# Optimization experiments

Measured on AMD Instinct MI355X. Metric: run time of the kernel, lower is better.

The kernel has to match this reference:

```python
import jax, jax.numpy as jnp
import numpy as np
from math import sqrt

B, L = 2, 1024
D, H, NL, DFF = 768, 12, 2, 3072
V, LCTX, EOS = 50257, 1024, 50256
STD = 0.02


def _ln(x, w, b, eps=1e-5):
    m = x.mean(-1, keepdims=True)
    v = ((x - m) ** 2).mean(-1, keepdims=True)
    return (x - m) * jax.lax.rsqrt(v + eps) * w + b


def setup_inputs() -> dict:
    key = jax.random.key(0)
    ks = jax.random.split(key, 12)
    ids = jax.random.randint(ks[0], (B, L), 0, V)
    # insert eos tokens so the packed-document mask has real segments
    ids = ids.at[:, 255::256].set(EOS)
    n = lambda k, s: STD * jax.random.normal(k, s, jnp.float32)
    return {
        "input_ids": ids,
        "tok_emb": n(ks[1], (V, D)),
        "pos_emb": n(ks[2], (LCTX, D)),
        "qkv_w": n(ks[3], (NL, 3 * D, D)),
        "qkv_b": jnp.zeros((NL, 3 * D), jnp.float32),
        "out_w": n(ks[4], (NL, D, D)),
        "out_b": jnp.zeros((NL, D), jnp.float32),
        "ln1_w": jnp.ones((NL, D), jnp.float32),
        "ln1_b": jnp.zeros((NL, D), jnp.float32),
        "ln2_w": jnp.ones((NL, D), jnp.float32),
        "ln2_b": jnp.zeros((NL, D), jnp.float32),
        "ff1_w": n(ks[5], (NL, DFF, D)),
        "ff1_b": jnp.zeros((NL, DFF), jnp.float32),
        "ff2_w": n(ks[6], (NL, D, DFF)),
        "ff2_b": jnp.zeros((NL, D), jnp.float32),
    }


def _supporters(input_ids):
    # relative position within document + per-batch additive segment-causal mask
    raw = jnp.arange(L)[None, :]                                   # [1,L]
    is_eos = input_ids == EOS
    last_eos = jax.lax.cummax(jnp.where(is_eos, raw, 0), axis=1)   # [B,L]
    rel_idx = raw - last_eos                                       # [B,L]
    seg = jnp.cumsum(is_eos.astype(jnp.int32), axis=1)             # [B,L]
    same = seg[:, :, None] == seg[:, None, :]                      # [B,L,L]
    causal = jnp.tril(jnp.ones((L, L), bool))
    mask = jnp.where(same & causal, 0.0, -jnp.inf).astype(jnp.float32)
    return rel_idx, mask


def _forward(input_ids, tok_emb, pos_emb, qkv_w, qkv_b, out_w, out_b,
             ln1_w, ln1_b, ln2_w, ln2_b, ff1_w, ff1_b, ff2_w, ff2_b):
    rel_idx, mask = _supporters(input_ids)
    x = tok_emb[input_ids] * sqrt(D) + pos_emb[rel_idx]            # [B,L,D]
    hd = D // H
    scale = 1.0 / sqrt(hd)

    def layer(x, p):
        (qw, qb, ow, ob, l1w, l1b, l2w, l2b, f1w, f1b, f2w, f2b) = p
        qkv = x @ qw.T + qb                                        # [B,L,3D]
        q, k, v = jnp.split(qkv, 3, axis=-1)
        q = q.reshape(B, L, H, hd)
        k = k.reshape(B, L, H, hd)
        v = v.reshape(B, L, H, hd)
        scores = jnp.einsum("bqhd,bkhd->bhqk", q, k) * scale + mask[:, None]
        attn = jax.nn.softmax(scores, axis=-1)
        o = jnp.einsum("bhqk,bkhd->bqhd", attn, v).reshape(B, L, D)
        o = o @ ow.T + ob
        x = _ln(x + o, l1w, l1b)                                   # post-norm
        h = jax.nn.gelu(x @ f1w.T + f1b, approximate=False) @ f2w.T + f2b
        x = _ln(x + h, l2w, l2b)
        return x, None

    x, _ = jax.lax.scan(layer, x, (qkv_w, qkv_b, out_w, out_b, ln1_w, ln1_b,
                                   ln2_w, ln2_b, ff1_w, ff1_b, ff2_w, ff2_b))
    return x @ tok_emb.T                                           # tied decoder


def reference(input_ids, tok_emb, pos_emb, qkv_w, qkv_b, out_w, out_b,
              ln1_w, ln1_b, ln2_w, ln2_b, ff1_w, ff1_b, ff2_w, ff2_b):
    return _forward(input_ids, tok_emb, pos_emb, qkv_w, qkv_b, out_w, out_b,
                    ln1_w, ln1_b, ln2_w, ln2_b, ff1_w, ff1_b, ff2_w, ff2_b)
```

## Files before the change

kernel.cpp:

```cpp
#include <hip/hip_runtime.h>
#include <hip/hip_bf16.h>

#define B_ 2
#define L_ 1024
#define D_ 768
#define H_ 12
#define HD_ 64
#define NL_ 2
#define DFF_ 3072
#define V_ 50257
#define EOS_ 50256
#define TD_ (3 * D_)
#define BL_ (B_ * L_)

typedef __attribute__((ext_vector_type(8))) short bf16x8_t;
typedef __attribute__((ext_vector_type(4))) float f32x4_t;

#define AS1 __attribute__((address_space(1)))
#define AS3 __attribute__((address_space(3)))

__device__ __forceinline__ unsigned short f2bf(float f) {
  union { float f; unsigned int i; } c;
  c.f = f;
  unsigned int x = c.i;
  unsigned int lsb = (x >> 16) & 1u;
  x += 0x7fffu + lsb;
  return (unsigned short)(x >> 16);
}

__device__ __forceinline__ void gload_lds16(const void* g, void* l) {
  __builtin_amdgcn_global_load_lds((AS1 void*)(g), (AS3 void*)(l), 16, 0, 0);
}

__global__ void cvt_kernel(const float* __restrict__ in,
                           unsigned short* __restrict__ out, int n4) {
  int i = blockIdx.x * blockDim.x + threadIdx.x;
  if (i >= n4) return;
  f32x4_t v = *(const f32x4_t*)(in + (size_t)i * 4);
  ushort4 o;
  o.x = f2bf(v[0]); o.y = f2bf(v[1]); o.z = f2bf(v[2]); o.w = f2bf(v[3]);
  *(ushort4*)(out + (size_t)i * 4) = o;
}

__global__ void prep_kernel(const int* __restrict__ ids, int* __restrict__ rel) {
  int i = blockIdx.x * blockDim.x + threadIdx.x;
  if (i >= BL_) return;
  int b = i / L_, l = i % L_;
  const int* row = ids + (size_t)b * L_;
  int r = l;
  for (int j = l; j >= 0; --j) {
    if (row[j] == EOS_) { r = l - j; break; }
  }
  rel[i] = r;
}

__global__ void embed_kernel(const int* __restrict__ ids,
                             const float* __restrict__ tok,
                             const float* __restrict__ pos,
                             const int* __restrict__ rel,
                             float* __restrict__ x,
                             unsigned short* __restrict__ xb) {
  int i = blockIdx.x * blockDim.x + threadIdx.x;
  if (i >= BL_ * D_) return;
  int d = i % D_;
  int bl = i / D_;
  int id = ids[bl];
  int r = rel[bl];
  float val = tok[(size_t)id * D_ + d] * 27.712812921102035f +
              pos[(size_t)r * D_ + d];
  x[i] = val;
  xb[i] = f2bf(val);
}

__global__ __launch_bounds__(256) void gemm_bt_lds_kernel(
    const unsigned short* __restrict__ A, const unsigned short* __restrict__ W,
    const float* __restrict__ bias, float* __restrict__ C,
    int M, int N, int K) {
  __shared__ unsigned short As[128 * 64];
  __shared__ unsigned short Bs[128 * 64];

  const int tid = threadIdx.x;
  const int wave = tid >> 6;
  const int lane = tid & 63;
  const int wr = wave >> 1;
  const int wc = wave & 1;
  const int lr = lane & 15;
  const int kq = (lane >> 4) << 3;

  const int nwg = gridDim.x * gridDim.y;
  const int bidl = blockIdx.y * gridDim.x + blockIdx.x;
  const int xcd = bidl & 7;
  const int q8 = nwg >> 3, r8 = nwg & 7;
  const int lin = (xcd < r8 ? xcd * (q8 + 1)
                            : r8 * (q8 + 1) + (xcd - r8) * q8) + (bidl >> 3);
  const int m0 = (lin % gridDim.x) << 7;
  const int n0 = (lin / gridDim.x) << 7;

  const int srow = tid >> 3;
  const int slot = tid & 7;
  const unsigned short* gA[4];
  const unsigned short* gB[4];
#pragma unroll
  for (int p = 0; p < 4; ++p) {
    int row = p * 32 + srow;
    int kblk = (slot ^ (row & 7)) << 3;
    gA[p] = A + (size_t)(m0 + row) * K + kblk;
    int wrow = n0 + row;
    if (wrow >= N) wrow = N - 1;
    gB[p] = W + (size_t)wrow * K + kblk;
  }

  f32x4_t acc[4][4];
#pragma unroll
  for (int i = 0; i < 4; ++i)
#pragma unroll
    for (int j = 0; j < 4; ++j) acc[i][j] = (f32x4_t){0.f, 0.f, 0.f, 0.f};

  const int xmask = (lr & 7) << 4;
  const char* Ab = (const char*)As;
  const char* Bb = (const char*)Bs;

  for (int k0 = 0; k0 < K; k0 += 64) {
    if (k0) __syncthreads();
#pragma unroll
    for (int p = 0; p < 4; ++p) {
      gload_lds16(gA[p] + k0, (char*)As + p * 4096 + wave * 1024);
      gload_lds16(gB[p] + k0, (char*)Bs + p * 4096 + wave * 1024);
    }
    __syncthreads();
#pragma unroll
    for (int ks = 0; ks < 2; ++ks) {
      const int kb = (ks << 6) + (kq << 1);
      bf16x8_t a[4], b[4];
#pragma unroll
      for (int i = 0; i < 4; ++i)
        a[i] = *(const bf16x8_t*)(Ab + (wr * 64 + i * 16 + lr) * 128 +
                                  (kb ^ xmask));
#pragma unroll
      for (int j = 0; j < 4; ++j)
        b[j] = *(const bf16x8_t*)(Bb + (wc * 64 + j * 16 + lr) * 128 +
                                  (kb ^ xmask));
#pragma unroll
      for (int i = 0; i < 4; ++i)
#pragma unroll
        for (int j = 0; j < 4; ++j)
          acc[i][j] =
              __builtin_amdgcn_mfma_f32_16x16x32_bf16(a[i], b[j], acc[i][j],
                                                      0, 0, 0);
    }
  }

  const int crow0 = m0 + wr * 64 + ((lane >> 4) << 2);
#pragma unroll
  for (int i = 0; i < 4; ++i) {
    int crow = crow0 + i * 16;
#pragma unroll
    for (int j = 0; j < 4; ++j) {
      int col = n0 + wc * 64 + j * 16 + lr;
      if (col >= N) continue;
      float bv = bias ? bias[col] : 0.0f;
#pragma unroll
      for (int r = 0; r < 4; ++r)
        C[(size_t)(crow + r) * N + col] = acc[i][j][r] + bv;
    }
  }
}

template <int W_IS_F32>
__global__ __launch_bounds__(256) void gemm_bt_kernel(
    const unsigned short* __restrict__ A, const void* __restrict__ W,
    const float* __restrict__ bias, float* __restrict__ C,
    int M, int N, int K) {
  int wave = threadIdx.x >> 6;
  int lane = threadIdx.x & 63;
  int lr = lane & 15;
  int kq = (lane >> 4) << 3;
  int n0 = blockIdx.x << 6;
  int m0 = blockIdx.y << 6;
  int row = m0 + wave * 16 + lr;

  const unsigned short* arow = A + (size_t)row * K + kq;
  const unsigned short* browb[4];
  const float* browf[4];
#pragma unroll
  for (int nt = 0; nt < 4; ++nt) {
    int col = n0 + nt * 16 + lr;
    if (col >= N) col = N - 1;
    if (W_IS_F32) browf[nt] = (const float*)W + (size_t)col * K + kq;
    else          browb[nt] = (const unsigned short*)W + (size_t)col * K + kq;
  }

  f32x4_t acc[4] = {{0.f, 0.f, 0.f, 0.f},
                    {0.f, 0.f, 0.f, 0.f},
                    {0.f, 0.f, 0.f, 0.f},
                    {0.f, 0.f, 0.f, 0.f}};

  for (int k0 = 0; k0 < K; k0 += 32) {
    bf16x8_t a = *(const bf16x8_t*)(arow + k0);
#pragma unroll
    for (int nt = 0; nt < 4; ++nt) {
      bf16x8_t bfr;
      if (W_IS_F32) {
        f32x4_t w0 = *(const f32x4_t*)(browf[nt] + k0);
        f32x4_t w1 = *(const f32x4_t*)(browf[nt] + k0 + 4);
#pragma unroll
        for (int j = 0; j < 4; ++j) {
          bfr[j]     = (short)f2bf(w0[j]);
          bfr[4 + j] = (short)f2bf(w1[j]);
        }
      } else {
        bfr = *(const bf16x8_t*)(browb[nt] + k0);
      }
      acc[nt] = __builtin_amdgcn_mfma_f32_16x16x32_bf16(a, bfr, acc[nt], 0, 0, 0);
    }
  }

  int crow = m0 + wave * 16 + ((lane >> 4) << 2);
#pragma unroll
  for (int nt = 0; nt < 4; ++nt) {
    int col = n0 + nt * 16 + lr;
    if (col >= N) continue;
    float bv = bias ? bias[col] : 0.0f;
#pragma unroll
    for (int r = 0; r < 4; ++r) {
      float v = acc[nt][r] + bv;
      C[(size_t)(crow + r) * N + col] = v;
    }
  }
}

__global__ __launch_bounds__(256) void attn_mfma_kernel(
    const float* __restrict__ qkv, const int* __restrict__ rel,
    unsigned short* __restrict__ obf) {
  __shared__ __align__(16) unsigned short k_s[64][72];
  __shared__ __align__(16) unsigned short v_s[64][72];
  __shared__ __align__(16) unsigned short p_s[4][16][72];

  const int tid = threadIdx.x;
  const int wave = tid >> 6, lane = tid & 63;
  const int lr = lane & 15, hi = lane >> 4;

  const int bid = blockIdx.x;
  const int qt0 = (bid & 15) << 6;
  const int h = (bid >> 4) % H_;
  const int b = bid / (16 * H_);
  const int boff = b * L_;

  const int qrow = qt0 + wave * 16 + lr;
  const float* qp = qkv + (size_t)(boff + qrow) * TD_ + h * HD_ + hi * 8;
  bf16x8_t aq[2];
#pragma unroll
  for (int ks = 0; ks < 2; ++ks) {
    f32x4_t q0 = *(const f32x4_t*)(qp + ks * 32);
    f32x4_t q1 = *(const f32x4_t*)(qp + ks * 32 + 4);
#pragma unroll
    for (int j = 0; j < 4; ++j) {
      aq[ks][j] = (short)f2bf(q0[j]);
      aq[ks][4 + j] = (short)f2bf(q1[j]);
    }
  }

  int klo_r[4];
#pragma unroll
  for (int r = 0; r < 4; ++r) {
    int qr = qt0 + wave * 16 + hi * 4 + r;
    klo_r[r] = qr - rel[boff + qr];
  }
  const int base0 = ((qt0 - rel[boff + qt0]) >> 6) << 6;

  float m_r[4] = {-1e30f, -1e30f, -1e30f, -1e30f};
  float l_r[4] = {0.f, 0.f, 0.f, 0.f};
  f32x4_t o_acc[4];
#pragma unroll
  for (int dt = 0; dt < 4; ++dt) o_acc[dt] = (f32x4_t){0.f, 0.f, 0.f, 0.f};

  const int skey = tid >> 2;
  const int sdq = (tid & 3) << 4;

  for (int base = base0; base <= qt0 + 63; base += 64) {
    __syncthreads();
    const float* kp = qkv + (size_t)(boff + base + skey) * TD_ + D_ +
                      h * HD_ + sdq;
    f32x4_t k0 = *(const f32x4_t*)(kp);
    f32x4_t k1 = *(const f32x4_t*)(kp + 4);
    f32x4_t k2 = *(const f32x4_t*)(kp + 8);
    f32x4_t k3 = *(const f32x4_t*)(kp + 12);
    bf16x8_t kb0, kb1;
#pragma unroll
    for (int j = 0; j < 4; ++j) {
      kb0[j] = (short)f2bf(k0[j]); kb0[4 + j] = (short)f2bf(k1[j]);
      kb1[j] = (short)f2bf(k2[j]); kb1[4 + j] = (short)f2bf(k3[j]);
    }
    *(bf16x8_t*)&k_s[skey][sdq] = kb0;
    *(bf16x8_t*)&k_s[skey][sdq + 8] = kb1;

    const float* vp = kp + D_;
    f32x4_t v0 = *(const f32x4_t*)(vp);
    f32x4_t v1 = *(const f32x4_t*)(vp + 4);
    f32x4_t v2 = *(const f32x4_t*)(vp + 8);
    f32x4_t v3 = *(const f32x4_t*)(vp + 12);
#pragma unroll
    for (int j = 0; j < 4; ++j) {
      v_s[sdq + j][skey]      = f2bf(v0[j]);
      v_s[sdq + 4 + j][skey]  = f2bf(v1[j]);
      v_s[sdq + 8 + j][skey]  = f2bf(v2[j]);
      v_s[sdq + 12 + j][skey] = f2bf(v3[j]);
    }
    __syncthreads();

    f32x4_t s[4];
#pragma unroll
    for (int tj = 0; tj < 4; ++tj) {
      s[tj] = (f32x4_t){0.f, 0.f, 0.f, 0.f};
#pragma unroll
      for (int ks = 0; ks < 2; ++ks) {
        bf16x8_t kb = *(const bf16x8_t*)&k_s[tj * 16 + lr][ks * 32 + hi * 8];
        s[tj] = __builtin_amdgcn_mfma_f32_16x16x32_bf16(aq[ks], kb, s[tj],
                                                        0, 0, 0);
      }
    }

    float al_r[4];
#pragma unroll
    for (int r = 0; r < 4; ++r) {
      const int qr = qt0 + wave * 16 + hi * 4 + r;
#pragma unroll
      for (int tj = 0; tj < 4; ++tj) {
        int key = base + tj * 16 + lr;
        bool valid = (key >= klo_r[r]) && (key <= qr);
        s[tj][r] = valid ? s[tj][r] * 0.125f : -1e30f;
      }
      float cm = fmaxf(fmaxf(s[0][r], s[1][r]), fmaxf(s[2][r], s[3][r]));
#pragma unroll
      for (int off = 8; off; off >>= 1)
        cm = fmaxf(cm, __shfl_xor(cm, off, 64));
      float mn = fmaxf(m_r[r], cm);
      al_r[r] = __expf(m_r[r] - mn);
      float rs = 0.f;
#pragma unroll
      for (int tj = 0; tj < 4; ++tj) {
        float p = (s[tj][r] < -1e29f) ? 0.f : __expf(s[tj][r] - mn);
        s[tj][r] = p;
        rs += p;
      }
#pragma unroll
      for (int off = 8; off; off >>= 1) rs += __shfl_xor(rs, off, 64);
      l_r[r] = l_r[r] * al_r[r] + rs;
      m_r[r] = mn;
    }

#pragma unroll
    for (int r = 0; r < 4; ++r) {
#pragma unroll
      for (int tj = 0; tj < 4; ++tj)
        p_s[wave][hi * 4 + r][tj * 16 + lr] = f2bf(s[tj][r]);
#pragma unroll
      for (int dt = 0; dt < 4; ++dt) o_acc[dt][r] *= al_r[r];
    }

#pragma unroll
    for (int ks = 0; ks < 2; ++ks) {
      bf16x8_t pa = *(const bf16x8_t*)&p_s[wave][lr][ks * 32 + hi * 8];
#pragma unroll
      for (int dt = 0; dt < 4; ++dt) {
        bf16x8_t vb = *(const bf16x8_t*)&v_s[dt * 16 + lr][ks * 32 + hi * 8];
        o_acc[dt] = __builtin_amdgcn_mfma_f32_16x16x32_bf16(pa, vb, o_acc[dt],
                                                            0, 0, 0);
      }
    }
  }

#pragma unroll
  for (int r = 0; r < 4; ++r) {
    float inv = 1.f / l_r[r];
    int qr = qt0 + wave * 16 + hi * 4 + r;
    unsigned short* op = obf + (size_t)(boff + qr) * D_ + h * HD_ + lr;
#pragma unroll
    for (int dt = 0; dt < 4; ++dt)
      op[dt * 16] = f2bf(o_acc[dt][r] * inv);
  }
}

__device__ __forceinline__ float block_reduce_sum_256(float v, float* sbuf) {
#pragma unroll
  for (int off = 32; off; off >>= 1) v += __shfl_xor(v, off, 64);
  if ((threadIdx.x & 63) == 0) sbuf[threadIdx.x >> 6] = v;
  __syncthreads();
  float r = sbuf[0] + sbuf[1] + sbuf[2] + sbuf[3];
  __syncthreads();
  return r;
}

__global__ __launch_bounds__(256) void add_ln_kernel(
    const float* __restrict__ x, const float* __restrict__ t,
    const float* __restrict__ w, const float* __restrict__ b,
    float* __restrict__ xo, unsigned short* __restrict__ xbo) {
  __shared__ float sbuf[4];
  size_t base = (size_t)blockIdx.x * D_;
  float v[3];
  float s = 0.f;
#pragma unroll
  for (int i = 0; i < 3; ++i) {
    int idx = threadIdx.x + i * 256;
    v[i] = x[base + idx] + t[base + idx];
    s += v[i];
  }
  float mean = block_reduce_sum_256(s, sbuf) * (1.f / D_);
  float vs = 0.f;
#pragma unroll
  for (int i = 0; i < 3; ++i) {
    float d = v[i] - mean;
    vs += d * d;
  }
  float var = block_reduce_sum_256(vs, sbuf) * (1.f / D_);
  float rstd = rsqrtf(var + 1e-5f);
#pragma unroll
  for (int i = 0; i < 3; ++i) {
    int idx = threadIdx.x + i * 256;
    float o = (v[i] - mean) * rstd * w[idx] + b[idx];
    xo[base + idx] = o;
    xbo[base + idx] = f2bf(o);
  }
}

__global__ void gelu_kernel(const float* __restrict__ h,
                            unsigned short* __restrict__ hb, int n) {
  int i = blockIdx.x * blockDim.x + threadIdx.x;
  if (i >= n) return;
  float x = h[i];
  float g = 0.5f * x * (1.f + erff(x * 0.7071067811865476f));
  hb[i] = f2bf(g);
}

extern "C" void kernel_launch(void* const* d_in, const int* in_sizes, int n_in,
                              void* d_out, int out_size, void* d_ws, size_t ws_size,
                              hipStream_t stream) {
  const int* ids       = (const int*)d_in[0];
  const float* tok     = (const float*)d_in[1];
  const float* pos     = (const float*)d_in[2];
  const float* qkv_w   = (const float*)d_in[3];
  const float* qkv_b   = (const float*)d_in[4];
  const float* out_w   = (const float*)d_in[5];
  const float* out_b   = (const float*)d_in[6];
  const float* ln1_w   = (const float*)d_in[7];
  const float* ln1_b   = (const float*)d_in[8];
  const float* ln2_w   = (const float*)d_in[9];
  const float* ln2_b   = (const float*)d_in[10];
  const float* ff1_w   = (const float*)d_in[11];
  const float* ff2_w   = (const float*)d_in[13];
  const float* ff2_b   = (const float*)d_in[14];
  const float* ff1_b   = (const float*)d_in[12];

  char* ws = (char*)d_ws;
  size_t off = 0;
  auto alloc = [&](size_t bytes) {
    void* p = ws + off;
    off = (off + bytes + 255) & ~(size_t)255;
    return p;
  };
  int* rel            = (int*)alloc((size_t)BL_ * 4);
  float* x            = (float*)alloc((size_t)BL_ * D_ * 4);
  unsigned short* xb  = (unsigned short*)alloc((size_t)BL_ * D_ * 2);
  float* big          = (float*)alloc((size_t)BL_ * DFF_ * 4);
  float* qkvbuf       = big;
  float* hbuf         = big;
  unsigned short* obf = (unsigned short*)alloc((size_t)BL_ * D_ * 2);
  float* t            = (float*)alloc((size_t)BL_ * D_ * 4);
  unsigned short* hb  = (unsigned short*)alloc((size_t)BL_ * DFF_ * 2);
  unsigned short* qkvw_b16 = (unsigned short*)alloc((size_t)NL_ * TD_ * D_ * 2);
  unsigned short* outw_b16 = (unsigned short*)alloc((size_t)NL_ * D_ * D_ * 2);
  unsigned short* ff1w_b16 = (unsigned short*)alloc((size_t)NL_ * DFF_ * D_ * 2);
  unsigned short* ff2w_b16 = (unsigned short*)alloc((size_t)NL_ * D_ * DFF_ * 2);
  size_t base_need = off;
  unsigned short* tok_b16 = (unsigned short*)alloc((size_t)V_ * D_ * 2);
  bool have_tok = (off <= ws_size);
  (void)base_need;

  auto cvt = [&](const float* in, unsigned short* out, size_t n) {
    int n4 = (int)(n / 4);
    cvt_kernel<<<(n4 + 255) / 256, 256, 0, stream>>>(in, out, n4);
  };
  cvt(qkv_w, qkvw_b16, (size_t)NL_ * TD_ * D_);
  cvt(out_w, outw_b16, (size_t)NL_ * D_ * D_);
  cvt(ff1_w, ff1w_b16, (size_t)NL_ * DFF_ * D_);
  cvt(ff2_w, ff2w_b16, (size_t)NL_ * D_ * DFF_);
  if (have_tok) cvt(tok, tok_b16, (size_t)V_ * D_);

  prep_kernel<<<(BL_ + 255) / 256, 256, 0, stream>>>(ids, rel);
  embed_kernel<<<(BL_ * D_ + 255) / 256, 256, 0, stream>>>(ids, tok, pos, rel, x, xb);

  auto gemm = [&](const unsigned short* A, const unsigned short* W,
                  const float* bias, float* C, int M, int N, int K) {
    gemm_bt_lds_kernel<<<dim3(M / 128, (N + 127) / 128), 256, 0, stream>>>(
        A, W, bias, C, M, N, K);
  };

  for (int l = 0; l < NL_; ++l) {
    gemm(xb, qkvw_b16 + (size_t)l * TD_ * D_, qkv_b + (size_t)l * TD_, qkvbuf,
         BL_, TD_, D_);
    attn_mfma_kernel<<<B_ * H_ * (L_ / 64), 256, 0, stream>>>(qkvbuf, rel, obf);
    gemm(obf, outw_b16 + (size_t)l * D_ * D_, out_b + (size_t)l * D_, t,
         BL_, D_, D_);
    add_ln_kernel<<<BL_, 256, 0, stream>>>(x, t, ln1_w + l * D_, ln1_b + l * D_, x, xb);
    gemm(xb, ff1w_b16 + (size_t)l * DFF_ * D_, ff1_b + (size_t)l * DFF_, hbuf,
         BL_, DFF_, D_);
    gelu_kernel<<<(BL_ * DFF_ + 255) / 256, 256, 0, stream>>>(hbuf, hb, BL_ * DFF_);
    gemm(hb, ff2w_b16 + (size_t)l * D_ * DFF_, ff2_b + (size_t)l * D_, t,
         BL_, D_, DFF_);
    add_ln_kernel<<<BL_, 256, 0, stream>>>(x, t, ln2_w + l * D_, ln2_b + l * D_, x, xb);
  }

  if (have_tok) {
    gemm(xb, tok_b16, nullptr, (float*)d_out, BL_, V_, D_);
  } else {
    gemm_bt_kernel<1><<<dim3((V_ + 63) / 64, BL_ / 64), 256, 0, stream>>>(
        xb, tok, nullptr, (float*)d_out, BL_, V_, D_);
  }
}
```

Baseline: 1.204 ms.

## Double-buffer LDS tiles in bf16 GEMM and fuse GELU into FF1 epilogue

The LDS GEMM now keeps two shared-memory buffers and issues the global-to-LDS loads for the next K tile before computing on the current one, waiting with vmcnt so memory latency overlaps the MFMA work. Separately, the FF1 GEMM applies exact GELU in its epilogue and writes bf16 directly, which removes the standalone gelu kernel and the fp32 round trip of the hidden activations. The cost is doubled LDS per block (64KB), which may reduce occupancy. The hand-written waitcnt and barriers also depend on the load count per stage staying correct.

```diff
diff --git a/kernel.cpp b/kernel.cpp
--- a/kernel.cpp
+++ b/kernel.cpp
@@ -72,12 +72,13 @@
   xb[i] = f2bf(val);
 }
 
+template <int ACT>
 __global__ __launch_bounds__(256) void gemm_bt_lds_kernel(
     const unsigned short* __restrict__ A, const unsigned short* __restrict__ W,
-    const float* __restrict__ bias, float* __restrict__ C,
+    const float* __restrict__ bias, void* __restrict__ Cv,
     int M, int N, int K) {
-  __shared__ unsigned short As[128 * 64];
-  __shared__ unsigned short Bs[128 * 64];
+  __shared__ unsigned short As[2][128 * 64];
+  __shared__ unsigned short Bs[2][128 * 64];
 
   const int tid = threadIdx.x;
   const int wave = tid >> 6;
@@ -117,17 +118,30 @@
     for (int j = 0; j < 4; ++j) acc[i][j] = (f32x4_t){0.f, 0.f, 0.f, 0.f};
 
   const int xmask = (lr & 7) << 4;
-  const char* Ab = (const char*)As;
-  const char* Bb = (const char*)Bs;
-
-  for (int k0 = 0; k0 < K; k0 += 64) {
-    if (k0) __syncthreads();
+  const int NKT = K >> 6;
+
+  auto stage = [&](int buf, int kt) {
+    const int k0 = kt << 6;
 #pragma unroll
     for (int p = 0; p < 4; ++p) {
-      gload_lds16(gA[p] + k0, (char*)As + p * 4096 + wave * 1024);
-      gload_lds16(gB[p] + k0, (char*)Bs + p * 4096 + wave * 1024);
-    }
-    __syncthreads();
+      gload_lds16(gA[p] + k0, (char*)As[buf] + p * 4096 + wave * 1024);
+      gload_lds16(gB[p] + k0, (char*)Bs[buf] + p * 4096 + wave * 1024);
+    }
+  };
+
+  stage(0, 0);
+  int cur = 0;
+  for (int kt = 0; kt < NKT; ++kt) {
+    if (kt + 1 < NKT) {
+      stage(cur ^ 1, kt + 1);
+      asm volatile("s_waitcnt vmcnt(8)" ::: "memory");
+    } else {
+      asm volatile("s_waitcnt vmcnt(0)" ::: "memory");
+    }
+    __builtin_amdgcn_s_barrier();
+    __builtin_amdgcn_sched_barrier(0);
+    const char* Ab = (const char*)As[cur];
+    const char* Bb = (const char*)Bs[cur];
 #pragma unroll
     for (int ks = 0; ks < 2; ++ks) {
       const int kb = (ks << 6) + (kq << 1);
@@ -148,6 +162,9 @@
               __builtin_amdgcn_mfma_f32_16x16x32_bf16(a[i], b[j], acc[i][j],
                                                       0, 0, 0);
     }
+    __builtin_amdgcn_sched_barrier(0);
+    __builtin_amdgcn_s_barrier();
+    cur ^= 1;
   }
 
   const int crow0 = m0 + wr * 64 + ((lane >> 4) << 2);
@@ -160,8 +177,15 @@
       if (col >= N) continue;
       float bv = bias ? bias[col] : 0.0f;
 #pragma unroll
-      for (int r = 0; r < 4; ++r)
-        C[(size_t)(crow + r) * N + col] = acc[i][j][r] + bv;
+      for (int r = 0; r < 4; ++r) {
+        float v = acc[i][j][r] + bv;
+        if (ACT == 0) {
+          ((float*)Cv)[(size_t)(crow + r) * N + col] = v;
+        } else {
+          float g = 0.5f * v * (1.f + erff(v * 0.7071067811865476f));
+          ((unsigned short*)Cv)[(size_t)(crow + r) * N + col] = f2bf(g);
+        }
+      }
     }
   }
 }
@@ -421,15 +445,6 @@
     xo[base + idx] = o;
     xbo[base + idx] = f2bf(o);
   }
-}
-
-__global__ void gelu_kernel(const float* __restrict__ h,
-                            unsigned short* __restrict__ hb, int n) {
-  int i = blockIdx.x * blockDim.x + threadIdx.x;
-  if (i >= n) return;
-  float x = h[i];
-  float g = 0.5f * x * (1.f + erff(x * 0.7071067811865476f));
-  hb[i] = f2bf(g);
 }
 
 extern "C" void kernel_launch(void* const* d_in, const int* in_sizes, int n_in,
@@ -463,7 +478,6 @@
   unsigned short* xb  = (unsigned short*)alloc((size_t)BL_ * D_ * 2);
   float* big          = (float*)alloc((size_t)BL_ * DFF_ * 4);
   float* qkvbuf       = big;
-  float* hbuf         = big;
   unsigned short* obf = (unsigned short*)alloc((size_t)BL_ * D_ * 2);
   float* t            = (float*)alloc((size_t)BL_ * D_ * 4);
   unsigned short* hb  = (unsigned short*)alloc((size_t)BL_ * DFF_ * 2);
@@ -491,8 +505,8 @@
 
   auto gemm = [&](const unsigned short* A, const unsigned short* W,
                   const float* bias, float* C, int M, int N, int K) {
-    gemm_bt_lds_kernel<<<dim3(M / 128, (N + 127) / 128), 256, 0, stream>>>(
-        A, W, bias, C, M, N, K);
+    gemm_bt_lds_kernel<0><<<dim3(M / 128, (N + 127) / 128), 256, 0, stream>>>(
+        A, W, bias, (void*)C, M, N, K);
   };
 
   for (int l = 0; l < NL_; ++l) {
@@ -502,9 +516,9 @@
     gemm(obf, outw_b16 + (size_t)l * D_ * D_, out_b + (size_t)l * D_, t,
          BL_, D_, D_);
     add_ln_kernel<<<BL_, 256, 0, stream>>>(x, t, ln1_w + l * D_, ln1_b + l * D_, x, xb);
-    gemm(xb, ff1w_b16 + (size_t)l * DFF_ * D_, ff1_b + (size_t)l * DFF_, hbuf,
-         BL_, DFF_, D_);
-    gelu_kernel<<<(BL_ * DFF_ + 255) / 256, 256, 0, stream>>>(hbuf, hb, BL_ * DFF_);
+    gemm_bt_lds_kernel<1><<<dim3(BL_ / 128, DFF_ / 128), 256, 0, stream>>>(
+        xb, ff1w_b16 + (size_t)l * DFF_ * D_, ff1_b + (size_t)l * DFF_,
+        (void*)hb, BL_, DFF_, D_);
     gemm(hb, ff2w_b16 + (size_t)l * D_ * DFF_, ff2_b + (size_t)l * D_, t,
          BL_, D_, DFF_);
     add_ln_kernel<<<BL_, 256, 0, stream>>>(x, t, ln2_w + l * D_, ln2_b + l * D_, x, xb);
```

Measured after the change: 1.262 ms. 1.05x slower.

## Template GEMM tiles, fuse GELU into FF1 epilogue, nontemporal logits stores

Applied to the files above, without the earlier changes.

Templates the LDS GEMM on tile size, activation, and store type. It adds 64x64 tiles for small-N GEMMs (out-proj, FF2) so more workgroups fill the GPU. GELU is fused into the FF1 epilogue, writing bf16 directly, which removes the fp32 intermediate and the separate gelu pass. The large vocab logits GEMM uses nontemporal stores to avoid cache pollution. Smaller tiles lower data reuse per block, and erf in the epilogue adds compute to the GEMM tail.

```diff
diff --git a/kernel.cpp b/kernel.cpp
--- a/kernel.cpp
+++ b/kernel.cpp
@@ -72,12 +72,16 @@
   xb[i] = f2bf(val);
 }
 
-__global__ __launch_bounds__(256) void gemm_bt_lds_kernel(
+template <int BM, int BN, int ACT, int NT>
+__global__ __launch_bounds__(256) void gemm_tile_kernel(
     const unsigned short* __restrict__ A, const unsigned short* __restrict__ W,
-    const float* __restrict__ bias, float* __restrict__ C,
+    const float* __restrict__ bias, void* __restrict__ Cv,
     int M, int N, int K) {
-  __shared__ unsigned short As[128 * 64];
-  __shared__ unsigned short Bs[128 * 64];
+  constexpr int WTM = BM / 2, WTN = BN / 2;
+  constexpr int FM = WTM / 16, FN = WTN / 16;
+  constexpr int PA = BM / 32, PB = BN / 32;
+  __shared__ unsigned short As[BM * 64];
+  __shared__ unsigned short Bs[BN * 64];
 
   const int tid = threadIdx.x;
   const int wave = tid >> 6;
@@ -93,28 +97,33 @@
   const int q8 = nwg >> 3, r8 = nwg & 7;
   const int lin = (xcd < r8 ? xcd * (q8 + 1)
                             : r8 * (q8 + 1) + (xcd - r8) * q8) + (bidl >> 3);
-  const int m0 = (lin % gridDim.x) << 7;
-  const int n0 = (lin / gridDim.x) << 7;
+  const int m0 = (lin % gridDim.x) * BM;
+  const int n0 = (lin / gridDim.x) * BN;
 
   const int srow = tid >> 3;
   const int slot = tid & 7;
-  const unsigned short* gA[4];
-  const unsigned short* gB[4];
-#pragma unroll
-  for (int p = 0; p < 4; ++p) {
+  const unsigned short* gA[PA];
+  const unsigned short* gB[PB];
+#pragma unroll
+  for (int p = 0; p < PA; ++p) {
     int row = p * 32 + srow;
     int kblk = (slot ^ (row & 7)) << 3;
     gA[p] = A + (size_t)(m0 + row) * K + kblk;
+  }
+#pragma unroll
+  for (int p = 0; p < PB; ++p) {
+    int row = p * 32 + srow;
+    int kblk = (slot ^ (row & 7)) << 3;
     int wrow = n0 + row;
     if (wrow >= N) wrow = N - 1;
     gB[p] = W + (size_t)wrow * K + kblk;
   }
 
-  f32x4_t acc[4][4];
-#pragma unroll
-  for (int i = 0; i < 4; ++i)
-#pragma unroll
-    for (int j = 0; j < 4; ++j) acc[i][j] = (f32x4_t){0.f, 0.f, 0.f, 0.f};
+  f32x4_t acc[FM][FN];
+#pragma unroll
+  for (int i = 0; i < FM; ++i)
+#pragma unroll
+    for (int j = 0; j < FN; ++j) acc[i][j] = (f32x4_t){0.f, 0.f, 0.f, 0.f};
 
   const int xmask = (lr & 7) << 4;
   const char* Ab = (const char*)As;
@@ -123,45 +132,55 @@
   for (int k0 = 0; k0 < K; k0 += 64) {
     if (k0) __syncthreads();
 #pragma unroll
-    for (int p = 0; p < 4; ++p) {
+    for (int p = 0; p < PA; ++p)
       gload_lds16(gA[p] + k0, (char*)As + p * 4096 + wave * 1024);
+#pragma unroll
+    for (int p = 0; p < PB; ++p)
       gload_lds16(gB[p] + k0, (char*)Bs + p * 4096 + wave * 1024);
-    }
     __syncthreads();
 #pragma unroll
     for (int ks = 0; ks < 2; ++ks) {
       const int kb = (ks << 6) + (kq << 1);
-      bf16x8_t a[4], b[4];
-#pragma unroll
-      for (int i = 0; i < 4; ++i)
-        a[i] = *(const bf16x8_t*)(Ab + (wr * 64 + i * 16 + lr) * 128 +
+      bf16x8_t a[FM], b[FN];
+#pragma unroll
+      for (int i = 0; i < FM; ++i)
+        a[i] = *(const bf16x8_t*)(Ab + (wr * WTM + i * 16 + lr) * 128 +
                                   (kb ^ xmask));
 #pragma unroll
-      for (int j = 0; j < 4; ++j)
-        b[j] = *(const bf16x8_t*)(Bb + (wc * 64 + j * 16 + lr) * 128 +
+      for (int j = 0; j < FN; ++j)
+        b[j] = *(const bf16x8_t*)(Bb + (wc * WTN + j * 16 + lr) * 128 +
                                   (kb ^ xmask));
 #pragma unroll
-      for (int i = 0; i < 4; ++i)
-#pragma unroll
-        for (int j = 0; j < 4; ++j)
+      for (int i = 0; i < FM; ++i)
+#pragma unroll
+        for (int j = 0; j < FN; ++j)
           acc[i][j] =
               __builtin_amdgcn_mfma_f32_16x16x32_bf16(a[i], b[j], acc[i][j],
                                                       0, 0, 0);
     }
   }
 
-  const int crow0 = m0 + wr * 64 + ((lane >> 4) << 2);
-#pragma unroll
-  for (int i = 0; i < 4; ++i) {
+  const int crow0 = m0 + wr * WTM + ((lane >> 4) << 2);
+#pragma unroll
+  for (int i = 0; i < FM; ++i) {
     int crow = crow0 + i * 16;
 #pragma unroll
-    for (int j = 0; j < 4; ++j) {
-      int col = n0 + wc * 64 + j * 16 + lr;
+    for (int j = 0; j < FN; ++j) {
+      int col = n0 + wc * WTN + j * 16 + lr;
       if (col >= N) continue;
       float bv = bias ? bias[col] : 0.0f;
 #pragma unroll
-      for (int r = 0; r < 4; ++r)
-        C[(size_t)(crow + r) * N + col] = acc[i][j][r] + bv;
+      for (int r = 0; r < 4; ++r) {
+        float v = acc[i][j][r] + bv;
+        if (ACT == 0) {
+          float* cp = (float*)Cv + (size_t)(crow + r) * N + col;
+          if (NT) __builtin_nontemporal_store(v, cp);
+          else *cp = v;
+        } else {
+          float g = 0.5f * v * (1.f + erff(v * 0.7071067811865476f));
+          ((unsigned short*)Cv)[(size_t)(crow + r) * N + col] = f2bf(g);
+        }
+      }
     }
   }
 }
@@ -421,15 +440,6 @@
     xo[base + idx] = o;
     xbo[base + idx] = f2bf(o);
   }
-}
-
-__global__ void gelu_kernel(const float* __restrict__ h,
-                            unsigned short* __restrict__ hb, int n) {
-  int i = blockIdx.x * blockDim.x + threadIdx.x;
-  if (i >= n) return;
-  float x = h[i];
-  float g = 0.5f * x * (1.f + erff(x * 0.7071067811865476f));
-  hb[i] = f2bf(g);
 }
 
 extern "C" void kernel_launch(void* const* d_in, const int* in_sizes, int n_in,
@@ -463,7 +473,6 @@
   unsigned short* xb  = (unsigned short*)alloc((size_t)BL_ * D_ * 2);
   float* big          = (float*)alloc((size_t)BL_ * DFF_ * 4);
   float* qkvbuf       = big;
-  float* hbuf         = big;
   unsigned short* obf = (unsigned short*)alloc((size_t)BL_ * D_ * 2);
   float* t            = (float*)alloc((size_t)BL_ * D_ * 4);
   unsigned short* hb  = (unsigned short*)alloc((size_t)BL_ * DFF_ * 2);
@@ -491,8 +500,16 @@
 
   auto gemm = [&](const unsigned short* A, const unsigned short* W,
                   const float* bias, float* C, int M, int N, int K) {
-    gemm_bt_lds_kernel<<<dim3(M / 128, (N + 127) / 128), 256, 0, stream>>>(
-        A, W, bias, C, M, N, K);
+    int blocks128 = (M / 128) * ((N + 127) / 128);
+    if ((N % 64) == 0 && blocks128 < 384) {
+      gemm_tile_kernel<64, 64, 0, 0>
+          <<<dim3(M / 64, N / 64), 256, 0, stream>>>(A, W, bias, (void*)C,
+                                                     M, N, K);
+    } else {
+      gemm_tile_kernel<128, 128, 0, 0>
+          <<<dim3(M / 128, (N + 127) / 128), 256, 0, stream>>>(
+              A, W, bias, (void*)C, M, N, K);
+    }
   };
 
   for (int l = 0; l < NL_; ++l) {
@@ -502,16 +519,19 @@
     gemm(obf, outw_b16 + (size_t)l * D_ * D_, out_b + (size_t)l * D_, t,
          BL_, D_, D_);
     add_ln_kernel<<<BL_, 256, 0, stream>>>(x, t, ln1_w + l * D_, ln1_b + l * D_, x, xb);
-    gemm(xb, ff1w_b16 + (size_t)l * DFF_ * D_, ff1_b + (size_t)l * DFF_, hbuf,
-         BL_, DFF_, D_);
-    gelu_kernel<<<(BL_ * DFF_ + 255) / 256, 256, 0, stream>>>(hbuf, hb, BL_ * DFF_);
+    gemm_tile_kernel<128, 128, 1, 0>
+        <<<dim3(BL_ / 128, DFF_ / 128), 256, 0, stream>>>(
+            xb, ff1w_b16 + (size_t)l * DFF_ * D_, ff1_b + (size_t)l * DFF_,
+            (void*)hb, BL_, DFF_, D_);
     gemm(hb, ff2w_b16 + (size_t)l * D_ * DFF_, ff2_b + (size_t)l * D_, t,
          BL_, D_, DFF_);
     add_ln_kernel<<<BL_, 256, 0, stream>>>(x, t, ln2_w + l * D_, ln2_b + l * D_, x, xb);
   }
 
   if (have_tok) {
-    gemm(xb, tok_b16, nullptr, (float*)d_out, BL_, V_, D_);
+    gemm_tile_kernel<128, 128, 0, 1>
+        <<<dim3(BL_ / 128, (V_ + 127) / 128), 256, 0, stream>>>(
+            xb, tok_b16, nullptr, (void*)d_out, BL_, V_, D_);
   } else {
     gemm_bt_kernel<1><<<dim3((V_ + 63) / 64, BL_ / 64), 256, 0, stream>>>(
         xb, tok, nullptr, (float*)d_out, BL_, V_, D_);
```

After: 1.312 ms. 1.09x slower.
